# Kernel tuning notes

Hardware: AMD Instinct MI355X
Metric: run time of the kernel (lower is better)

Reference implementation:

```python
import jax, jax.numpy as jnp
import numpy as np

B, N1, K, E, H = 64, 8, 128, 256, 512


def setup_inputs() -> dict:
    key = jax.random.key(0)
    ks = jax.random.split(key, 10)
    s = 1.0 / np.sqrt(E)
    sh = 1.0 / np.sqrt(H)
    return {
        "queries": jax.random.normal(ks[0], (B, N1, E), jnp.float32),
        "keys": jax.random.normal(ks[1], (B, N1, K, E), jnp.float32),
        "cum_subs_masks": jax.random.randint(ks[2], (B, N1, K, 1), 0, 2, jnp.int32),
        "num_neg": N1 - 1,
        "wk_w": jax.random.uniform(ks[3], (H, E), jnp.float32, -s, s),
        "wk_b": jax.random.uniform(ks[4], (H,), jnp.float32, -s, s),
        "wq_w": jax.random.uniform(ks[5], (H, E), jnp.float32, -s, s),
        "wq_b": jax.random.uniform(ks[6], (H,), jnp.float32, -s, s),
        "wv_w": jax.random.uniform(ks[7], (1, H), jnp.float32, -sh, sh),
        "wv_b": jax.random.uniform(ks[8], (1,), jnp.float32, -sh, sh),
    }


def reference(queries, keys, cum_subs_masks, num_neg, wk_w, wk_b, wq_w, wq_b, wv_w, wv_b):
    # queries: (B, N1, E) -> project and broadcast over keys dim
    q_proj = jnp.einsum("bne,he->bnh", queries, wq_w) + wq_b        # (B, N1, H)
    k_proj = jnp.einsum("bnke,he->bnkh", keys, wk_w) + wk_b          # (B, N1, K, H)
    hidden = jnp.tanh(q_proj[:, :, None, :] + k_proj)                # (B, N1, K, H)
    scores = jnp.einsum("bnkh,oh->bnko", hidden, wv_w) + wv_b        # (B, N1, K, 1)
    scores = scores + cum_subs_masks.astype(scores.dtype) * (-1e9)
    attn_weight = jax.nn.softmax(scores, axis=-2)                    # over K
    attn_out = jnp.sum(attn_weight * keys, axis=-2)                  # (B, N1, E)
    return attn_out, attn_weight
```

## Files before the change

### kernel.cpp

```cpp
#include <hip/hip_runtime.h>
#include <hip/hip_bf16.h>

#define B_  64
#define N1_ 8
#define KK  128
#define EE  256
#define HH  512
#define BN  (B_ * N1_)

typedef __attribute__((ext_vector_type(8))) short short8;
typedef __attribute__((ext_vector_type(4))) float f32x4;

__device__ __forceinline__ short bfs(float f) {
  __hip_bfloat16 h = __float2bfloat16(f);
  return __builtin_bit_cast(short, h);
}
__device__ __forceinline__ float bf2f(short s) {
  unsigned int u = ((unsigned int)(unsigned short)s) << 16;
  return __builtin_bit_cast(float, u);
}
__device__ __forceinline__ float tanhf_fast(float x) {
  float e2 = __builtin_amdgcn_exp2f(2.8853900817779268f * x);
  return 1.0f - 2.0f * __builtin_amdgcn_rcpf(e2 + 1.0f);
}

__global__ __launch_bounds__(256) void k_prep(
    const float* __restrict__ wk_w,
    const float* __restrict__ queries,
    const float* __restrict__ wq_w,
    const float* __restrict__ wq_b,
    const float* __restrict__ wk_b,
    unsigned short* __restrict__ wk_fr,
    float* __restrict__ qp) {
  const int bid = blockIdx.x, t = threadIdx.x;
  if (bid < 64) {
    const int g  = bid * 256 + t;
    const int h  = g >> 5;
    const int e0 = (g & 31) * 8;
    float4 x = *(const float4*)(wk_w + (size_t)h * EE + e0);
    float4 y = *(const float4*)(wk_w + (size_t)h * EE + e0 + 4);
    short8 f;
    f[0] = bfs(x.x); f[1] = bfs(x.y); f[2] = bfs(x.z); f[3] = bfs(x.w);
    f[4] = bfs(y.x); f[5] = bfs(y.y); f[6] = bfs(y.z); f[7] = bfs(y.w);
    const int ht = h >> 4, hl = h & 15;
    const int s = e0 >> 5, lg = (e0 >> 3) & 3;
    const int chunk = (ht * 8 + s) * 64 + lg * 16 + hl;
    *(short8*)(wk_fr + (size_t)chunk * 8) = f;
  } else {
    const int w = t >> 6, l = t & 63, lg = l >> 4, ll = l & 15;
    const int g2 = bid - 64;
    const int bn0 = (g2 >> 1) * 16;
    const int ht0 = (g2 & 1) * 16;
    short8 af[8];
    {
      const float* qr = queries + (size_t)(bn0 + ll) * EE + lg * 8;
      #pragma unroll
      for (int s = 0; s < 8; ++s) {
        float4 x = *(const float4*)(qr + s * 32);
        float4 y = *(const float4*)(qr + s * 32 + 4);
        short8 f;
        f[0] = bfs(x.x); f[1] = bfs(x.y); f[2] = bfs(x.z); f[3] = bfs(x.w);
        f[4] = bfs(y.x); f[5] = bfs(y.y); f[6] = bfs(y.z); f[7] = bfs(y.w);
        af[s] = f;
      }
    }
    #pragma unroll
    for (int i = 0; i < 4; ++i) {
      const int ht = ht0 + w * 4 + i;
      const float* bp = wq_w + (size_t)(ht * 16 + ll) * EE + lg * 8;
      f32x4 a = {0.f, 0.f, 0.f, 0.f};
      #pragma unroll
      for (int s = 0; s < 8; ++s) {
        float4 x = *(const float4*)(bp + s * 32);
        float4 y = *(const float4*)(bp + s * 32 + 4);
        short8 f;
        f[0] = bfs(x.x); f[1] = bfs(x.y); f[2] = bfs(x.z); f[3] = bfs(x.w);
        f[4] = bfs(y.x); f[5] = bfs(y.y); f[6] = bfs(y.z); f[7] = bfs(y.w);
        a = __builtin_amdgcn_mfma_f32_16x16x32_bf16(af[s], f, a, 0, 0, 0);
      }
      const int h = ht * 16 + ll;
      const float add = wq_b[h] + wk_b[h];
      #pragma unroll
      for (int r = 0; r < 4; ++r)
        qp[(size_t)(bn0 + lg * 4 + r) * HH + h] = a[r] + add;
    }
  }
}

__global__ __launch_bounds__(256, 2) void k_fused(
    const float* __restrict__ keys,
    const unsigned short* __restrict__ wk_fr,
    const float* __restrict__ wv_w,
    const float* __restrict__ qp,
    const int* __restrict__ masks,
    float* __restrict__ out) {
  const int t  = threadIdx.x;
  const int w  = t >> 6;
  const int l  = t & 63;
  const int lg = l >> 4;
  const int ll = l & 15;
  const int bn = blockIdx.x;

  __shared__ float2 qw_s[HH];
  __shared__ float sc[KK];
  __shared__ float red[2];
  __shared__ float po[4][256];

  {
    float2 v0; v0.x = qp[(size_t)bn * HH + t];       v0.y = wv_w[t];
    float2 v1; v1.x = qp[(size_t)bn * HH + t + 256]; v1.y = wv_w[t + 256];
    qw_s[t] = v0;
    qw_s[t + 256] = v1;
  }

  short8 af0[8], af1[8];
  {
    const float* kp0 = keys + (size_t)(bn * KK + w * 32 + ll) * EE + lg * 8;
    const float* kp1 = kp0 + 16 * EE;
    #pragma unroll
    for (int s = 0; s < 8; ++s) {
      float4 x = *(const float4*)(kp0 + s * 32);
      float4 y = *(const float4*)(kp0 + s * 32 + 4);
      short8 f;
      f[0] = bfs(x.x); f[1] = bfs(x.y); f[2] = bfs(x.z); f[3] = bfs(x.w);
      f[4] = bfs(y.x); f[5] = bfs(y.y); f[6] = bfs(y.z); f[7] = bfs(y.w);
      af0[s] = f;
      x = *(const float4*)(kp1 + s * 32);
      y = *(const float4*)(kp1 + s * 32 + 4);
      f[0] = bfs(x.x); f[1] = bfs(x.y); f[2] = bfs(x.z); f[3] = bfs(x.w);
      f[4] = bfs(y.x); f[5] = bfs(y.y); f[6] = bfs(y.z); f[7] = bfs(y.w);
      af1[s] = f;
    }
  }
  __syncthreads();

  const char* wkb = (const char*)wk_fr;
  const int lofs = l * 16;

  float p0[4] = {0.f, 0.f, 0.f, 0.f};
  float p1[4] = {0.f, 0.f, 0.f, 0.f};
  float4 A0, A1, A2, A3, A4, A5, A6, A7;
  float4 B0, B1, B2, B3, B4, B5, B6, B7;

#define ISSUE(b0,b1,b2,b3,b4,b5,b6,b7, ti) {                               \
    const char* p_ = wkb + (size_t)(ti) * 8192 + lofs;                     \
    const char* q_ = p_ + 4096;                                            \
    asm volatile(                                                          \
      "global_load_dwordx4 %0, %8, off\n\t"                                \
      "global_load_dwordx4 %1, %8, off offset:1024\n\t"                    \
      "global_load_dwordx4 %2, %8, off offset:2048\n\t"                    \
      "global_load_dwordx4 %3, %8, off offset:3072\n\t"                    \
      "global_load_dwordx4 %4, %9, off\n\t"                                \
      "global_load_dwordx4 %5, %9, off offset:1024\n\t"                    \
      "global_load_dwordx4 %6, %9, off offset:2048\n\t"                    \
      "global_load_dwordx4 %7, %9, off offset:3072"                        \
      : "=&v"(b0), "=&v"(b1), "=&v"(b2), "=&v"(b3),                        \
        "=&v"(b4), "=&v"(b5), "=&v"(b6), "=&v"(b7)                        \
      : "v"(p_), "v"(q_)); }

#define WAITV(n)  {                                                        \
    asm volatile("s_waitcnt vmcnt(" #n ")" ::: "memory");                  \
    __builtin_amdgcn_sched_barrier(0); }

#define COMPUTE(b0,b1,b2,b3,b4,b5,b6,b7, ii) {                             \
    f32x4 a0 = {0.f, 0.f, 0.f, 0.f};                                       \
    f32x4 a1 = {0.f, 0.f, 0.f, 0.f};                                       \
    short8 f_;                                                             \
    __builtin_amdgcn_s_setprio(1);                                         \
    f_ = __builtin_bit_cast(short8, b0);                                   \
    a0 = __builtin_amdgcn_mfma_f32_16x16x32_bf16(af0[0], f_, a0, 0, 0, 0); \
    a1 = __builtin_amdgcn_mfma_f32_16x16x32_bf16(af1[0], f_, a1, 0, 0, 0); \
    f_ = __builtin_bit_cast(short8, b1);                                   \
    a0 = __builtin_amdgcn_mfma_f32_16x16x32_bf16(af0[1], f_, a0, 0, 0, 0); \
    a1 = __builtin_amdgcn_mfma_f32_16x16x32_bf16(af1[1], f_, a1, 0, 0, 0); \
    f_ = __builtin_bit_cast(short8, b2);                                   \
    a0 = __builtin_amdgcn_mfma_f32_16x16x32_bf16(af0[2], f_, a0, 0, 0, 0); \
    a1 = __builtin_amdgcn_mfma_f32_16x16x32_bf16(af1[2], f_, a1, 0, 0, 0); \
    f_ = __builtin_bit_cast(short8, b3);                                   \
    a0 = __builtin_amdgcn_mfma_f32_16x16x32_bf16(af0[3], f_, a0, 0, 0, 0); \
    a1 = __builtin_amdgcn_mfma_f32_16x16x32_bf16(af1[3], f_, a1, 0, 0, 0); \
    f_ = __builtin_bit_cast(short8, b4);                                   \
    a0 = __builtin_amdgcn_mfma_f32_16x16x32_bf16(af0[4], f_, a0, 0, 0, 0); \
    a1 = __builtin_amdgcn_mfma_f32_16x16x32_bf16(af1[4], f_, a1, 0, 0, 0); \
    f_ = __builtin_bit_cast(short8, b5);                                   \
    a0 = __builtin_amdgcn_mfma_f32_16x16x32_bf16(af0[5], f_, a0, 0, 0, 0); \
    a1 = __builtin_amdgcn_mfma_f32_16x16x32_bf16(af1[5], f_, a1, 0, 0, 0); \
    f_ = __builtin_bit_cast(short8, b6);                                   \
    a0 = __builtin_amdgcn_mfma_f32_16x16x32_bf16(af0[6], f_, a0, 0, 0, 0); \
    a1 = __builtin_amdgcn_mfma_f32_16x16x32_bf16(af1[6], f_, a1, 0, 0, 0); \
    f_ = __builtin_bit_cast(short8, b7);                                   \
    a0 = __builtin_amdgcn_mfma_f32_16x16x32_bf16(af0[7], f_, a0, 0, 0, 0); \
    a1 = __builtin_amdgcn_mfma_f32_16x16x32_bf16(af1[7], f_, a1, 0, 0, 0); \
    __builtin_amdgcn_s_setprio(0);                                         \
    const float2 qw = qw_s[(ii) * 16 + ll];                                \
    _Pragma("unroll") for (int r = 0; r < 4; ++r) {                        \
      p0[r] += qw.y * tanhf_fast(a0[r] + qw.x);                            \
      p1[r] += qw.y * tanhf_fast(a1[r] + qw.x); } }

  ISSUE(A0,A1,A2,A3,A4,A5,A6,A7, 0);
  ISSUE(B0,B1,B2,B3,B4,B5,B6,B7, 1);
  #pragma unroll 1
  for (int i = 0; i < 30; i += 2) {
    WAITV(8);
    COMPUTE(A0,A1,A2,A3,A4,A5,A6,A7, i);
    ISSUE(A0,A1,A2,A3,A4,A5,A6,A7, i + 2);
    WAITV(8);
    COMPUTE(B0,B1,B2,B3,B4,B5,B6,B7, i + 1);
    ISSUE(B0,B1,B2,B3,B4,B5,B6,B7, i + 3);
  }
  WAITV(8);
  COMPUTE(A0,A1,A2,A3,A4,A5,A6,A7, 30);
  WAITV(0);
  COMPUTE(B0,B1,B2,B3,B4,B5,B6,B7, 31);
#undef COMPUTE
#undef WAITV
#undef ISSUE

  #pragma unroll
  for (int r = 0; r < 4; ++r) {
    #pragma unroll
    for (int off = 1; off <= 8; off <<= 1) {
      p0[r] += __shfl_xor(p0[r], off, 64);
      p1[r] += __shfl_xor(p1[r], off, 64);
    }
  }
  if (ll == 0) {
    #pragma unroll
    for (int r = 0; r < 4; ++r) {
      sc[w * 32 + lg * 4 + r]      = p0[r];
      sc[w * 32 + 16 + lg * 4 + r] = p1[r];
    }
  }
  __syncthreads();

  if (t < KK) sc[t] += (float)masks[bn * KK + t] * (-1e9f);
  __syncthreads();
  if (t < 64) {
    float a = fmaxf(sc[t], sc[t + 64]);
    #pragma unroll
    for (int off = 32; off >= 1; off >>= 1) a = fmaxf(a, __shfl_xor(a, off, 64));
    if (t == 0) red[0] = a;
  }
  __syncthreads();
  const float m = red[0];
  if (t < KK) sc[t] = expf(sc[t] - m);
  __syncthreads();
  if (t < 64) {
    float a = sc[t] + sc[t + 64];
    #pragma unroll
    for (int off = 32; off >= 1; off >>= 1) a += __shfl_xor(a, off, 64);
    if (t == 0) red[1] = a;
  }
  __syncthreads();
  const float inv = 1.f / red[1];
  if (t < KK) {
    float wgt = sc[t] * inv;
    sc[t] = wgt;
    out[BN * EE + (size_t)bn * KK + t] = wgt;
  }
  __syncthreads();

  {
    const float wgt0 = sc[w * 32 + ll];
    const float wgt1 = sc[w * 32 + 16 + ll];
    #pragma unroll
    for (int s = 0; s < 8; ++s) {
      float pv[8];
      #pragma unroll
      for (int j = 0; j < 8; ++j)
        pv[j] = wgt0 * bf2f(af0[s][j]) + wgt1 * bf2f(af1[s][j]);
      #pragma unroll
      for (int j = 0; j < 8; ++j) {
        #pragma unroll
        for (int off = 1; off <= 8; off <<= 1)
          pv[j] += __shfl_xor(pv[j], off, 64);
      }
      if (ll == 0) {
        float4 v0 = {pv[0], pv[1], pv[2], pv[3]};
        float4 v1 = {pv[4], pv[5], pv[6], pv[7]};
        *(float4*)(&po[w][lg * 8 + s * 32])     = v0;
        *(float4*)(&po[w][lg * 8 + s * 32 + 4]) = v1;
      }
    }
  }
  __syncthreads();
  out[(size_t)bn * EE + t] = po[0][t] + po[1][t] + po[2][t] + po[3][t];
}

extern "C" void kernel_launch(void* const* d_in, const int* in_sizes, int n_in,
                              void* d_out, int out_size, void* d_ws, size_t ws_size,
                              hipStream_t stream) {
  const float* queries = (const float*)d_in[0];
  const float* keys    = (const float*)d_in[1];
  const int*   masks   = (const int*)d_in[2];
  const float* wk_w = (const float*)d_in[4];
  const float* wk_b = (const float*)d_in[5];
  const float* wq_w = (const float*)d_in[6];
  const float* wq_b = (const float*)d_in[7];
  const float* wv_w = (const float*)d_in[8];

  float* out = (float*)d_out;
  float* qp  = (float*)d_ws;
  unsigned short* wk_fr = (unsigned short*)(qp + BN * HH);

  k_prep<<<128, 256, 0, stream>>>(wk_w, queries, wq_w, wq_b, wk_b, wk_fr, qp);
  k_fused<<<BN, 256, 0, stream>>>(keys, wk_fr, wv_w, qp, masks, out);
}
```

Measured before the change: 49.81 us.

## Stage Wk tiles cooperatively through double-buffered LDS instead of per-wave global loads

Before, each wave loaded the full 8 KB Wk fragment tile per H-tile directly from global memory into registers, so the four waves fetched the same data four times. Now the 256 threads load each tile once (two dwordx4 per thread), write it into a double-buffered shared array, and every wave reads its MFMA B fragments from LDS. This cuts redundant global/L2 traffic and the register pressure of sixteen in-flight float4s. In exchange it adds a block-wide barrier and an LDS round trip on every iteration, and the prefetch depth drops from two tiles to one.

```diff
diff --git a/kernel.cpp b/kernel.cpp
--- a/kernel.cpp
+++ b/kernel.cpp
@@ -101,6 +101,7 @@
   const int ll = l & 15;
   const int bn = blockIdx.x;
 
+  __shared__ __align__(16) char bsm[2][8192];
   __shared__ float2 qw_s[HH];
   __shared__ float sc[KK];
   __shared__ float red[2];
@@ -112,6 +113,27 @@
     qw_s[t] = v0;
     qw_s[t + 256] = v1;
   }
+
+  const char* wkb = (const char*)wk_fr;
+  float4 r0, r1;
+
+#define ISSUE(ti) {                                                        \
+    const char* p_ = wkb + (size_t)(ti) * 8192 + t * 16;                   \
+    const char* q_ = p_ + 4096;                                            \
+    asm volatile(                                                          \
+      "global_load_dwordx4 %0, %2, off\n\t"                                \
+      "global_load_dwordx4 %1, %3, off"                                    \
+      : "=&v"(r0), "=&v"(r1) : "v"(p_), "v"(q_)); }
+
+#define WAITV0 {                                                           \
+    asm volatile("s_waitcnt vmcnt(0)" ::: "memory");                       \
+    __builtin_amdgcn_sched_barrier(0); }
+
+#define DSWRITE(buf) {                                                     \
+    *(float4*)(&bsm[buf][t * 16])        = r0;                             \
+    *(float4*)(&bsm[buf][4096 + t * 16]) = r1; }
+
+  ISSUE(0);
 
   short8 af0[8], af1[8];
   {
@@ -132,88 +154,42 @@
       af1[s] = f;
     }
   }
-  __syncthreads();
-
-  const char* wkb = (const char*)wk_fr;
-  const int lofs = l * 16;
+  WAITV0;
+  DSWRITE(0);
+  __syncthreads();
 
   float p0[4] = {0.f, 0.f, 0.f, 0.f};
   float p1[4] = {0.f, 0.f, 0.f, 0.f};
-  float4 A0, A1, A2, A3, A4, A5, A6, A7;
-  float4 B0, B1, B2, B3, B4, B5, B6, B7;
-
-#define ISSUE(b0,b1,b2,b3,b4,b5,b6,b7, ti) {                               \
-    const char* p_ = wkb + (size_t)(ti) * 8192 + lofs;                     \
-    const char* q_ = p_ + 4096;                                            \
-    asm volatile(                                                          \
-      "global_load_dwordx4 %0, %8, off\n\t"                                \
-      "global_load_dwordx4 %1, %8, off offset:1024\n\t"                    \
-      "global_load_dwordx4 %2, %8, off offset:2048\n\t"                    \
-      "global_load_dwordx4 %3, %8, off offset:3072\n\t"                    \
-      "global_load_dwordx4 %4, %9, off\n\t"                                \
-      "global_load_dwordx4 %5, %9, off offset:1024\n\t"                    \
-      "global_load_dwordx4 %6, %9, off offset:2048\n\t"                    \
-      "global_load_dwordx4 %7, %9, off offset:3072"                        \
-      : "=&v"(b0), "=&v"(b1), "=&v"(b2), "=&v"(b3),                        \
-        "=&v"(b4), "=&v"(b5), "=&v"(b6), "=&v"(b7)                        \
-      : "v"(p_), "v"(q_)); }
-
-#define WAITV(n)  {                                                        \
-    asm volatile("s_waitcnt vmcnt(" #n ")" ::: "memory");                  \
-    __builtin_amdgcn_sched_barrier(0); }
-
-#define COMPUTE(b0,b1,b2,b3,b4,b5,b6,b7, ii) {                             \
+
+#define COMPUTE(buf, ii) {                                                 \
     f32x4 a0 = {0.f, 0.f, 0.f, 0.f};                                       \
     f32x4 a1 = {0.f, 0.f, 0.f, 0.f};                                       \
-    short8 f_;                                                             \
     __builtin_amdgcn_s_setprio(1);                                         \
-    f_ = __builtin_bit_cast(short8, b0);                                   \
-    a0 = __builtin_amdgcn_mfma_f32_16x16x32_bf16(af0[0], f_, a0, 0, 0, 0); \
-    a1 = __builtin_amdgcn_mfma_f32_16x16x32_bf16(af1[0], f_, a1, 0, 0, 0); \
-    f_ = __builtin_bit_cast(short8, b1);                                   \
-    a0 = __builtin_amdgcn_mfma_f32_16x16x32_bf16(af0[1], f_, a0, 0, 0, 0); \
-    a1 = __builtin_amdgcn_mfma_f32_16x16x32_bf16(af1[1], f_, a1, 0, 0, 0); \
-    f_ = __builtin_bit_cast(short8, b2);                                   \
-    a0 = __builtin_amdgcn_mfma_f32_16x16x32_bf16(af0[2], f_, a0, 0, 0, 0); \
-    a1 = __builtin_amdgcn_mfma_f32_16x16x32_bf16(af1[2], f_, a1, 0, 0, 0); \
-    f_ = __builtin_bit_cast(short8, b3);                                   \
-    a0 = __builtin_amdgcn_mfma_f32_16x16x32_bf16(af0[3], f_, a0, 0, 0, 0); \
-    a1 = __builtin_amdgcn_mfma_f32_16x16x32_bf16(af1[3], f_, a1, 0, 0, 0); \
-    f_ = __builtin_bit_cast(short8, b4);                                   \
-    a0 = __builtin_amdgcn_mfma_f32_16x16x32_bf16(af0[4], f_, a0, 0, 0, 0); \
-    a1 = __builtin_amdgcn_mfma_f32_16x16x32_bf16(af1[4], f_, a1, 0, 0, 0); \
-    f_ = __builtin_bit_cast(short8, b5);                                   \
-    a0 = __builtin_amdgcn_mfma_f32_16x16x32_bf16(af0[5], f_, a0, 0, 0, 0); \
-    a1 = __builtin_amdgcn_mfma_f32_16x16x32_bf16(af1[5], f_, a1, 0, 0, 0); \
-    f_ = __builtin_bit_cast(short8, b6);                                   \
-    a0 = __builtin_amdgcn_mfma_f32_16x16x32_bf16(af0[6], f_, a0, 0, 0, 0); \
-    a1 = __builtin_amdgcn_mfma_f32_16x16x32_bf16(af1[6], f_, a1, 0, 0, 0); \
-    f_ = __builtin_bit_cast(short8, b7);                                   \
-    a0 = __builtin_amdgcn_mfma_f32_16x16x32_bf16(af0[7], f_, a0, 0, 0, 0); \
-    a1 = __builtin_amdgcn_mfma_f32_16x16x32_bf16(af1[7], f_, a1, 0, 0, 0); \
+    _Pragma("unroll") for (int s = 0; s < 8; ++s) {                        \
+      short8 bfr = *(const short8*)(&bsm[buf][s * 1024 + l * 16]);         \
+      a0 = __builtin_amdgcn_mfma_f32_16x16x32_bf16(af0[s], bfr, a0, 0, 0, 0); \
+      a1 = __builtin_amdgcn_mfma_f32_16x16x32_bf16(af1[s], bfr, a1, 0, 0, 0); \
+    }                                                                      \
     __builtin_amdgcn_s_setprio(0);                                         \
     const float2 qw = qw_s[(ii) * 16 + ll];                                \
     _Pragma("unroll") for (int r = 0; r < 4; ++r) {                        \
       p0[r] += qw.y * tanhf_fast(a0[r] + qw.x);                            \
       p1[r] += qw.y * tanhf_fast(a1[r] + qw.x); } }
 
-  ISSUE(A0,A1,A2,A3,A4,A5,A6,A7, 0);
-  ISSUE(B0,B1,B2,B3,B4,B5,B6,B7, 1);
   #pragma unroll 1
-  for (int i = 0; i < 30; i += 2) {
-    WAITV(8);
-    COMPUTE(A0,A1,A2,A3,A4,A5,A6,A7, i);
-    ISSUE(A0,A1,A2,A3,A4,A5,A6,A7, i + 2);
-    WAITV(8);
-    COMPUTE(B0,B1,B2,B3,B4,B5,B6,B7, i + 1);
-    ISSUE(B0,B1,B2,B3,B4,B5,B6,B7, i + 3);
-  }
-  WAITV(8);
-  COMPUTE(A0,A1,A2,A3,A4,A5,A6,A7, 30);
-  WAITV(0);
-  COMPUTE(B0,B1,B2,B3,B4,B5,B6,B7, 31);
+  for (int i = 0; i < 32; ++i) {
+    if (i < 31) ISSUE(i + 1);
+    COMPUTE(i & 1, i);
+    if (i < 31) {
+      WAITV0;
+      DSWRITE((i + 1) & 1);
+    }
+    asm volatile("s_waitcnt lgkmcnt(0)" ::: "memory");
+    __builtin_amdgcn_s_barrier();
+  }
 #undef COMPUTE
-#undef WAITV
+#undef DSWRITE
+#undef WAITV0
 #undef ISSUE
 
   #pragma unroll
```

Result: slower. 53.33 us (+7.1%).
